# Optimization experiments

Measured on AMD Instinct MI355X. Metric: run time of the kernel, lower is better.

Reference implementation:

```python
import jax, jax.numpy as jnp
import numpy as np
from jax import lax

DIM = 768
SLICES = 12
HEADS = 16
P = 8                      # window_size
CS = DIM // SLICES         # channels per group = 64
HD = DIM // HEADS          # head_dim = 48
BLK = HD // SLICES         # mask block = 4


def group_norm(x, w, b, groups, eps=1e-5):
    # torch GroupNorm: normalize over (C//groups, H, W) per group, biased var
    B, C, H, W = x.shape
    xg = x.reshape(B, groups, (C // groups) * H * W)
    mu = xg.mean(axis=2, keepdims=True)
    var = xg.var(axis=2, keepdims=True)
    xn = ((xg - mu) * lax.rsqrt(var + eps)).reshape(B, C, H, W)
    return xn * w[None, :, None, None] + b[None, :, None, None]


def gconv1x1(x, w, b, groups):
    # grouped 1x1 conv == block-diagonal matmul over channel groups
    B, C, H, W = x.shape
    Co = w.shape[0]
    xg = x.reshape(B, groups, C // groups, H * W)
    wg = w.reshape(groups, Co // groups, C // groups)
    out = jnp.einsum('goi,bgin->bgon', wg, xg).reshape(B, Co, H, W)
    return out + b[None, :, None, None]


def dwconv3(x, w, b):
    # depthwise 3x3, padding 1 (SAME)
    out = lax.conv_general_dilated(x, w, (1, 1), 'SAME',
                                   feature_group_count=x.shape[1],
                                   dimension_numbers=('NCHW', 'OIHW', 'NCHW'))
    return out + b[None, :, None, None]


def gelu(x):
    return jax.nn.gelu(x, approximate=False)  # torch nn.GELU default = exact erf


def tca_forward(y, norm1_w, norm1_b, cpe_w, cpe_b, cpe_nw, cpe_nb,
                qw, qb, kw, kb, vw, vb, pw, pb,
                norm2_w, norm2_b, f1w, f1b, f2w, f2b):
    B, C, H, W = y.shape
    w1, w2 = H // P, W // P
    # window partition: b c (w1 p1) (w2 p2) -> (b w1 w2) c p1 p2
    yw = y.reshape(B, C, w1, P, w2, P).transpose(0, 2, 4, 1, 3, 5).reshape(B * w1 * w2, C, P, P)
    yn = group_norm(yw, norm1_w, norm1_b, SLICES)
    # ConvPosEnc: x + gelu(groupnorm(dwconv(x)))
    feat = group_norm(dwconv3(yn, cpe_w, cpe_b), cpe_nw, cpe_nb, SLICES)
    yn = yn + gelu(feat)
    q = gconv1x1(yn, qw, qb, SLICES)
    k = gconv1x1(yn, kw, kb, SLICES)
    v = gconv1x1(yn, vw, vb, SLICES)
    Bp = yn.shape[0]
    N = P * P
    # torch view(B,N,C//h,h): channel c = d*HEADS + head  ->  (Bp, HD, HEADS, N)
    def split(t):
        return t.reshape(Bp, HD, HEADS, N).transpose(0, 2, 1, 3)  # (Bp, h, hd, N)
    qh, kh, vh = split(q), split(k), split(v)
    scale = HD ** -0.5
    attn = jnp.einsum('bhdn,bhen->bhde', qh * scale, kh)  # channel-attention: (hd x hd)
    idx = jnp.arange(HD)
    mask = (idx[None, :] // BLK) > (idx[:, None] // BLK)  # block-causal over channel slices
    attn = jnp.where(mask[None, None], -jnp.inf, attn)
    attn = jax.nn.softmax(attn, axis=-1)
    out = jnp.einsum('bhde,bhen->bhdn', attn, vh)
    out = out.transpose(0, 2, 1, 3).reshape(Bp, C, P, P)  # back to c = d*HEADS + head
    out = gconv1x1(out, pw, pb, SLICES)
    # window reverse
    out = out.reshape(B, w1, w2, C, P, P).transpose(0, 3, 1, 4, 2, 5).reshape(B, C, H, W)
    tgt = y + out
    t2 = group_norm(tgt, norm2_w, norm2_b, SLICES)
    t2 = gconv1x1(gelu(gconv1x1(t2, f1w, f1b, SLICES)), f2w, f2b, SLICES)
    return tgt + t2


def setup_inputs():
    key = jax.random.key(0)
    ks = jax.random.split(key, 9)
    B, H, W = 2, 256, 256
    f32 = jnp.float32
    d = {}
    d['y'] = jax.random.normal(ks[0], (B, DIM, H, W), f32)
    d['norm1_w'] = jnp.ones((DIM,), f32); d['norm1_b'] = jnp.zeros((DIM,), f32)
    d['cpe_w'] = jax.random.normal(ks[1], (DIM, 1, 3, 3), f32) * 0.1
    d['cpe_b'] = jnp.zeros((DIM,), f32)
    d['cpe_nw'] = jnp.ones((DIM,), f32); d['cpe_nb'] = jnp.zeros((DIM,), f32)
    d['qw'] = jax.random.normal(ks[2], (DIM, CS), f32) * 0.05; d['qb'] = jnp.zeros((DIM,), f32)
    d['kw'] = jax.random.normal(ks[3], (DIM, CS), f32) * 0.05; d['kb'] = jnp.zeros((DIM,), f32)
    d['vw'] = jax.random.normal(ks[4], (DIM, CS), f32) * 0.05; d['vb'] = jnp.zeros((DIM,), f32)
    d['pw'] = jax.random.normal(ks[5], (DIM, CS), f32) * 0.05; d['pb'] = jnp.zeros((DIM,), f32)
    d['norm2_w'] = jnp.ones((DIM,), f32); d['norm2_b'] = jnp.zeros((DIM,), f32)
    d['f1w'] = jax.random.normal(ks[6], (DIM, CS), f32) * 0.05; d['f1b'] = jnp.zeros((DIM,), f32)
    d['f2w'] = jax.random.normal(ks[7], (DIM, CS), f32) * 0.05; d['f2b'] = jnp.zeros((DIM,), f32)
    return d


def reference(y, norm1_w, norm1_b, cpe_w, cpe_b, cpe_nw, cpe_nb,
              qw, qb, kw, kb, vw, vb, pw, pb,
              norm2_w, norm2_b, f1w, f1b, f2w, f2b):
    return tca_forward(y, norm1_w, norm1_b, cpe_w, cpe_b, cpe_nw, cpe_nb,
                       qw, qb, kw, kb, vw, vb, pw, pb,
                       norm2_w, norm2_b, f1w, f1b, f2w, f2b)
```

## Files before the change

kernel.cpp:

```cpp
#include <hip/hip_runtime.h>
#include <hip/hip_bf16.h>

#define IMG 256
#define NPOS 65536

typedef __attribute__((ext_vector_type(8))) short short8;
typedef __attribute__((ext_vector_type(4))) float f32x4;

__device__ __forceinline__ float gelu_exact(float x){
  return 0.5f * x * (1.0f + erff(x * 0.7071067811865475f));
}

__device__ __forceinline__ short f2b(float x){
  __hip_bfloat16 hh = __float2bfloat16(x);
  short s;
  __builtin_memcpy(&s, &hh, sizeof(s));
  return s;
}

__device__ __forceinline__ float b2f(short s){
  unsigned int u = ((unsigned int)(unsigned short)s) << 16;
  float f;
  __builtin_memcpy(&f, &u, sizeof(f));
  return f;
}

template<int NWAVES>
__device__ __forceinline__ void block_reduce2(float& s, float& s2, float* red){
  __syncthreads();
  #pragma unroll
  for (int off=32; off>0; off>>=1){ s += __shfl_down(s, off); s2 += __shfl_down(s2, off); }
  int lane = threadIdx.x & 63, w = threadIdx.x >> 6;
  if (lane==0){ red[w*2]=s; red[w*2+1]=s2; }
  __syncthreads();
  if (threadIdx.x==0){
    float a=0.f, bb=0.f;
    #pragma unroll
    for (int i=0;i<NWAVES;i++){ a+=red[i*2]; bb+=red[i*2+1]; }
    red[2*NWAVES]=a; red[2*NWAVES+1]=bb;
  }
  __syncthreads();
  s=red[2*NWAVES]; s2=red[2*NWAVES+1];
}

__global__ __launch_bounds__(1024) void w_cvt(
    const float* __restrict__ w0, const float* __restrict__ w1,
    const float* __restrict__ w2, const float* __restrict__ w3,
    const float* __restrict__ w4, const float* __restrict__ w5,
    short* __restrict__ outw)
{
  const int mi = blockIdx.y;
  const float* src = mi==0?w0: mi==1?w1: mi==2?w2: mi==3?w3: mi==4?w4: w5;
  const int i = blockIdx.x*1024 + threadIdx.x;
  outw[(size_t)mi*49152 + i] = f2b(src[i]);
}

__global__ __launch_bounds__(1024) void k_abcp(
    const float* __restrict__ y,
    const float* __restrict__ n1w, const float* __restrict__ n1b,
    const float* __restrict__ cw,  const float* __restrict__ cb,
    const float* __restrict__ cnw, const float* __restrict__ cnb,
    const short* __restrict__ qwB, const float* __restrict__ qb,
    const short* __restrict__ kwB, const float* __restrict__ kb,
    const short* __restrict__ vwB, const float* __restrict__ vb,
    const short* __restrict__ pwB, const float* __restrict__ pb,
    short* __restrict__ qG, short* __restrict__ kG, short* __restrict__ vG,
    float* __restrict__ out, float* __restrict__ part, int win0)
{
  extern __shared__ short SM[];
  char* SMb = (char*)SM;

  const int t = threadIdx.x;
  const int bid = blockIdx.x;
  const int nwq = gridDim.x >> 3;
  const int wl  = (bid & 7) * nwq + (bid >> 3);
  const int win = win0 + wl;
  const int b = win>>10, W1=(win>>5)&31, W2=win&31;
  const size_t ybase = (size_t)b*768*(size_t)NPOS + (size_t)(W1*8)*IMG + (W2*8);

  const int h = t>>6, ln = t&63;
  const int l15 = ln&15, c4 = ln>>4, kb8 = c4*8, rbase = c4*4;

  if (h < 12){
    const int g = h;
    const int p1 = ln>>3, p2 = ln&7;
    const bool up = p1>0, dn = p1<7, lt = p2>0, rt = p2<7;
    const float* yg = y + ybase + (size_t)(g*64)*NPOS + (size_t)p1*IMG + p2;
    const int swzofs = (ln&7)<<4;
    char* slotbase = SMb + ln*1536;

    float s=0.f, s2=0.f;
    #pragma unroll
    for (int c0=0;c0<64;c0+=8){
      short8 pk;
      #pragma unroll
      for (int j=0;j<8;++j){
        float v = yg[(size_t)(c0+j)*NPOS];
        s += v; s2 += v*v;
        pk[j] = f2b(v);
      }
      *(short8*)(slotbase + ((g*128 + c0*2) ^ swzofs)) = pk;
    }
    #pragma unroll
    for (int off=32; off>0; off>>=1){ s += __shfl_xor(s, off); s2 += __shfl_xor(s2, off); }
    const float mean = s * (1.f/4096.f);
    const float rstd = rsqrtf(s2*(1.f/4096.f) - mean*mean + 1e-5f);

    float sc=0.f, sc2=0.f;
    #pragma unroll 1
    for (int c0=0;c0<64;c0+=8){
      short8 y8 = *(const short8*)(slotbase + ((g*128 + c0*2) ^ swzofs));
      #pragma unroll
      for (int j=0;j<8;++j){
        const int cg = g*64 + c0 + j;
        float a = n1w[cg]*rstd;
        float x = fmaf(b2f(y8[j]), a, n1b[cg] - mean*a);
        float nmm = __shfl(x, (ln-9)&63);
        float nm0 = __shfl(x, (ln-8)&63);
        float nmp = __shfl(x, (ln-7)&63);
        float n0m = __shfl(x, (ln-1)&63);
        float n0p = __shfl(x, (ln+1)&63);
        float npm = __shfl(x, (ln+7)&63);
        float np0 = __shfl(x, (ln+8)&63);
        float npp = __shfl(x, (ln+9)&63);
        const float* wp = cw + cg*9;
        float acc = cb[cg];
        acc = fmaf(wp[0], (up&&lt)?nmm:0.f, acc);
        acc = fmaf(wp[1], up?nm0:0.f, acc);
        acc = fmaf(wp[2], (up&&rt)?nmp:0.f, acc);
        acc = fmaf(wp[3], lt?n0m:0.f, acc);
        acc = fmaf(wp[4], x, acc);
        acc = fmaf(wp[5], rt?n0p:0.f, acc);
        acc = fmaf(wp[6], (dn&&lt)?npm:0.f, acc);
        acc = fmaf(wp[7], dn?np0:0.f, acc);
        acc = fmaf(wp[8], (dn&&rt)?npp:0.f, acc);
        sc += acc; sc2 += acc*acc;
      }
    }
    #pragma unroll
    for (int off=32; off>0; off>>=1){ sc += __shfl_xor(sc, off); sc2 += __shfl_xor(sc2, off); }
    const float mean2 = sc * (1.f/4096.f);
    const float rstd2 = rsqrtf(sc2*(1.f/4096.f) - mean2*mean2 + 1e-5f);

    #pragma unroll 1
    for (int c0=0;c0<64;c0+=8){
      short8 y8 = *(const short8*)(slotbase + ((g*128 + c0*2) ^ swzofs));
      short8 o8;
      #pragma unroll
      for (int j=0;j<8;++j){
        const int cg = g*64 + c0 + j;
        float a = n1w[cg]*rstd;
        float x = fmaf(b2f(y8[j]), a, n1b[cg] - mean*a);
        float nmm = __shfl(x, (ln-9)&63);
        float nm0 = __shfl(x, (ln-8)&63);
        float nmp = __shfl(x, (ln-7)&63);
        float n0m = __shfl(x, (ln-1)&63);
        float n0p = __shfl(x, (ln+1)&63);
        float npm = __shfl(x, (ln+7)&63);
        float np0 = __shfl(x, (ln+8)&63);
        float npp = __shfl(x, (ln+9)&63);
        const float* wp = cw + cg*9;
        float acc = cb[cg];
        acc = fmaf(wp[0], (up&&lt)?nmm:0.f, acc);
        acc = fmaf(wp[1], up?nm0:0.f, acc);
        acc = fmaf(wp[2], (up&&rt)?nmp:0.f, acc);
        acc = fmaf(wp[3], lt?n0m:0.f, acc);
        acc = fmaf(wp[4], x, acc);
        acc = fmaf(wp[5], rt?n0p:0.f, acc);
        acc = fmaf(wp[6], (dn&&lt)?npm:0.f, acc);
        acc = fmaf(wp[7], dn?np0:0.f, acc);
        acc = fmaf(wp[8], (dn&&rt)?npp:0.f, acc);
        float f = (acc - mean2)*rstd2*cnw[cg] + cnb[cg];
        o8[j] = f2b(x + gelu_exact(f));
      }
      *(short8*)(slotbase + ((g*128 + c0*2) ^ swzofs)) = o8;
    }
  }
  __syncthreads();

  for (int u = h; u < 36; u += 16){
    const int mat = (u<12)?0:((u<24)?1:2);
    const int g = u - mat*12;
    const short* WB = mat==0?qwB:(mat==1?kwB:vwB);
    const float* Bb = mat==0?qb:(mat==1?kb:vb);
    short* dst = mat==0?qG:(mat==1?kG:vG);
    short8 afr[4][2];
    float bias[4][4];
    #pragma unroll
    for (int mt2=0;mt2<4;++mt2){
      #pragma unroll
      for (int ks=0;ks<2;++ks)
        afr[mt2][ks] = *(const short8*)&WB[(size_t)(g*64+mt2*16+l15)*64 + ks*32 + kb8];
      #pragma unroll
      for (int r=0;r<4;++r)
        bias[mt2][r] = Bb[g*64 + mt2*16 + rbase + r];
    }
    #pragma unroll
    for (int nt=0;nt<4;++nt){
      const int pos = nt*16 + l15;
      short8 b0 = *(const short8*)(SMb + pos*1536 + ((g*128 +      kb8*2) ^ ((pos&7)<<4)));
      short8 b1 = *(const short8*)(SMb + pos*1536 + ((g*128 + 64 + kb8*2) ^ ((pos&7)<<4)));
      #pragma unroll
      for (int mt2=0;mt2<4;++mt2){
        f32x4 acc = {0.f,0.f,0.f,0.f};
        acc = __builtin_amdgcn_mfma_f32_16x16x32_bf16(afr[mt2][0], b0, acc, 0,0,0);
        acc = __builtin_amdgcn_mfma_f32_16x16x32_bf16(afr[mt2][1], b1, acc, 0,0,0);
        #pragma unroll
        for (int r=0;r<4;++r){
          const int hh = rbase + r;
          float val = acc[r] + bias[mt2][r];
          size_t addr = ((size_t)(wl*16 + hh)*48 + 4*g + mt2)*64 + pos;
          dst[addr] = f2b(mat==0 ? val * 0.14433756729740643f : val);
        }
      }
    }
  }

  __threadfence_block();
  __syncthreads();

  const size_t hbase = (size_t)(wl*16+h)*48;
  short* R = SM + h*4096;

  short8 kf[3][2], qf[3][2];
  #pragma unroll
  for (int tt=0;tt<3;++tt)
    #pragma unroll
    for (int ks=0;ks<2;++ks){
      kf[tt][ks] = *(const short8*)&kG[(hbase + 16*tt + l15)*64 + ks*32 + kb8];
      qf[tt][ks] = *(const short8*)&qG[(hbase + 16*tt + l15)*64 + ks*32 + kb8];
    }
  f32x4 Su[6];
  const int DTa[6] = {0,1,1,2,2,2};
  const int ETa[6] = {0,0,1,0,1,2};
  #pragma unroll
  for (int u=0;u<6;++u){
    f32x4 acc = {0.f,0.f,0.f,0.f};
    acc = __builtin_amdgcn_mfma_f32_16x16x32_bf16(kf[ETa[u]][0], qf[DTa[u]][0], acc, 0,0,0);
    acc = __builtin_amdgcn_mfma_f32_16x16x32_bf16(kf[ETa[u]][1], qf[DTa[u]][1], acc, 0,0,0);
    Su[u] = acc;
  }

  float inv3[3];
  #pragma unroll
  for (int dt=0;dt<3;++dt){
    const int ub = (dt==0)?0:((dt==1)?1:3);
    float m = -1e30f;
    #pragma unroll
    for (int et=0; et<=dt; ++et)
      #pragma unroll
      for (int r=0;r<4;++r){
        bool valid = (et<dt) || ((rbase + r) <= (l15|3));
        if (valid) m = fmaxf(m, Su[ub+et][r]);
      }
    m = fmaxf(m, __shfl_xor(m,16));
    m = fmaxf(m, __shfl_xor(m,32));
    float sm = 0.f;
    #pragma unroll
    for (int et=0; et<=dt; ++et)
      #pragma unroll
      for (int r=0;r<4;++r){
        bool valid = (et<dt) || ((rbase + r) <= (l15|3));
        float p = valid ? expf(Su[ub+et][r] - m) : 0.f;
        Su[ub+et][r] = p; sm += p;
      }
    sm += __shfl_xor(sm,16);
    sm += __shfl_xor(sm,32);
    inv3[dt] = 1.f/sm;
  }

  short8 z8 = {0,0,0,0,0,0,0,0};
  #pragma unroll
  for (int nblk=0;nblk<8;++nblk){
    short8 v8 = z8;
    if (ln < 48) v8 = *(const short8*)&vG[(hbase + ln)*64 + nblk*8];
    #pragma unroll
    for (int j=0;j<8;++j){
      int n = nblk*8 + j;
      R[n*64 + (((ln>>3) ^ (n&7))<<3) + (ln&7)] = v8[j];
    }
  }
  short8 bv[4][2];
  #pragma unroll
  for (int nt=0;nt<4;++nt){
    const int n = 16*nt + l15;
    bv[nt][0] = *(const short8*)&R[n*64 + ((c4 ^ (n&7))<<3)];
    bv[nt][1] = *(const short8*)&R[n*64 + (((4+c4) ^ (n&7))<<3)];
  }

  #pragma unroll
  for (int i_=0;i_<6;++i_) *(short8*)&R[i_*512 + ln*8] = z8;
  #pragma unroll
  for (int dt=0;dt<3;++dt){
    const int ub = (dt==0)?0:((dt==1)?1:3);
    const int d = 16*dt + l15;
    #pragma unroll
    for (int et=0; et<=dt; ++et)
      #pragma unroll
      for (int r=0;r<4;++r){
        int e = 16*et + rbase + r;
        R[d*64 + (((e>>3) ^ (d&7))<<3) + (e&7)] = f2b(Su[ub+et][r]*inv3[dt]);
      }
  }
  short8 aP[4];
  const int PDT[4] = {0,1,2,2}, PKS[4] = {0,0,0,1};
  #pragma unroll
  for (int i_=0;i_<4;++i_){
    int d = 16*PDT[i_] + l15;
    int ch = PKS[i_]*4 + c4;
    aP[i_] = *(const short8*)&R[d*64 + ((ch ^ (d&7))<<3)];
  }

  __syncthreads();

  #pragma unroll
  for (int nt=0;nt<4;++nt){
    const int n = 16*nt + l15;
    f32x4 O0 = {0.f,0.f,0.f,0.f};
    f32x4 O1 = {0.f,0.f,0.f,0.f};
    f32x4 O2 = {0.f,0.f,0.f,0.f};
    O0 = __builtin_amdgcn_mfma_f32_16x16x32_bf16(aP[0], bv[nt][0], O0, 0,0,0);
    O1 = __builtin_amdgcn_mfma_f32_16x16x32_bf16(aP[1], bv[nt][0], O1, 0,0,0);
    O2 = __builtin_amdgcn_mfma_f32_16x16x32_bf16(aP[2], bv[nt][0], O2, 0,0,0);
    O2 = __builtin_amdgcn_mfma_f32_16x16x32_bf16(aP[3], bv[nt][1], O2, 0,0,0);
    #pragma unroll
    for (int r=0;r<4;++r){
      const int swz = (((2*r + (h>>3)) ^ (n&7))<<3) + (h&7);
      SM[(c4     )*4096 + n*64 + swz] = f2b(O0[r]);
      SM[(4 + c4 )*4096 + n*64 + swz] = f2b(O1[r]);
      SM[(8 + c4 )*4096 + n*64 + swz] = f2b(O2[r]);
    }
  }

  __syncthreads();

  #pragma unroll 1
  for (int j=0;j<3;++j){
    const int u = h*3 + j;
    const int g = u>>2, mt = u&3;
    short8 aw[2];
    float bi[4];
    #pragma unroll
    for (int ks=0;ks<2;++ks)
      aw[ks] = *(const short8*)&pwB[(size_t)(g*64 + mt*16 + l15)*64 + ks*32 + kb8];
    #pragma unroll
    for (int r=0;r<4;++r) bi[r] = pb[g*64 + mt*16 + rbase + r];

    f32x4 acc[4] = {};
    #pragma unroll
    for (int nt=0;nt<4;++nt){
      const int n = 16*nt + l15;
      short8 b0 = *(const short8*)&SM[g*4096 + n*64 + ((c4 ^ (n&7))<<3)];
      short8 b1 = *(const short8*)&SM[g*4096 + n*64 + (((4+c4) ^ (n&7))<<3)];
      acc[nt] = __builtin_amdgcn_mfma_f32_16x16x32_bf16(aw[0], b0, acc[nt], 0,0,0);
      acc[nt] = __builtin_amdgcn_mfma_f32_16x16x32_bf16(aw[1], b1, acc[nt], 0,0,0);
    }
    float s=0.f, s2=0.f;
    #pragma unroll
    for (int nt=0;nt<4;++nt){
      const int n = 16*nt + l15;
      const size_t rowoff = ybase + (size_t)(n>>3)*IMG + (n&7);
      #pragma unroll
      for (int r=0;r<4;++r){
        int m = mt*16 + rbase + r;
        size_t ad = rowoff + (size_t)(g*64+m)*NPOS;
        float o = y[ad] + bi[r] + acc[nt][r];
        out[ad] = o;
        s += o; s2 += o*o;
      }
    }
    #pragma unroll
    for (int off=32; off>0; off>>=1){ s += __shfl_xor(s, off); s2 += __shfl_xor(s2, off); }
    if (ln==0){
      size_t idx = ((size_t)(b*12+g)*1024 + (win&1023))*4 + mt;
      part[idx*2+0]=s; part[idx*2+1]=s2;
    }
  }
}

__global__ __launch_bounds__(256) void k3_stats(
    const float* __restrict__ part, float* __restrict__ stats)
{
  const int bg = blockIdx.x;
  const int t = threadIdx.x;
  float s=0.f, s2=0.f;
  #pragma unroll
  for (int j=0;j<16;++j){
    size_t idx = (size_t)bg*4096 + t*16 + j;
    s  += part[idx*2+0];
    s2 += part[idx*2+1];
  }
  __shared__ float red[10];
  block_reduce2<4>(s,s2,red);
  if (t==0){
    const float Ninv = 1.f/(64.f*65536.f);
    float mean = s*Ninv;
    float var  = s2*Ninv - mean*mean;
    stats[bg*2+0] = mean;
    stats[bg*2+1] = rsqrtf(var + 1e-5f);
  }
}

__global__ __launch_bounds__(256) void k_d(
    const float* __restrict__ n2w, const float* __restrict__ n2b,
    const short* __restrict__ f1wB, const float* __restrict__ f1b,
    const short* __restrict__ f2wB, const float* __restrict__ f2bi,
    const float* __restrict__ stats, float* __restrict__ io)
{
  __shared__ short Xb[4096];
  __shared__ short Hb[4096];
  const int t = threadIdx.x;
  const int pt = blockIdx.x, g = blockIdx.y, b = blockIdx.z;
  const int bg = b*12 + g;
  const float mean = stats[bg*2+0], rstd = stats[bg*2+1];
  const size_t base = ((size_t)(b*768 + g*64))*NPOS + (size_t)pt*64;

  const int wv = t>>6, ln = t&63;
  const int l15 = ln&15, kb8 = (ln>>4)*8, rbase = (ln>>4)*4, c4 = ln>>4;
  const int n = wv*16 + l15;

  float res[16];
  #pragma unroll
  for (int mt=0;mt<4;++mt)
    #pragma unroll
    for (int r=0;r<4;++r)
      res[mt*4+r] = io[base + (size_t)(mt*16 + rbase + r)*NPOS + n];

  {
    const int pp = t>>3, posq = t&7;
    const int ch0 = pp*2;
    const float* p0 = io + base + (size_t)ch0*NPOS + posq*8;
    float4 x00 = *(const float4*)p0;
    float4 x01 = *(const float4*)(p0+4);
    const float* p1 = p0 + NPOS;
    float4 x10 = *(const float4*)p1;
    float4 x11 = *(const float4*)(p1+4);
    float A0 = rstd*n2w[g*64+ch0],   C0 = n2b[g*64+ch0]   - mean*A0;
    float A1 = rstd*n2w[g*64+ch0+1], C1 = n2b[g*64+ch0+1] - mean*A1;
    float va[8] = {x00.x,x00.y,x00.z,x00.w,x01.x,x01.y,x01.z,x01.w};
    float vb[8] = {x10.x,x10.y,x10.z,x10.w,x11.x,x11.y,x11.z,x11.w};
    #pragma unroll
    for (int j=0;j<8;++j){
      int pos = posq*8 + j;
      unsigned int u0 = (unsigned short)f2b(va[j]*A0 + C0);
      unsigned int u1 = (unsigned short)f2b(vb[j]*A1 + C1);
      *(unsigned int*)&Xb[pos*64 + (((ch0>>3) ^ (pos&7))<<3) + (ch0&7)] = u0 | (u1<<16);
    }
  }
  __syncthreads();

  short8 af[4][2];
  #pragma unroll
  for (int mt=0;mt<4;++mt)
    #pragma unroll
    for (int ks=0;ks<2;++ks)
      af[mt][ks] = *(const short8*)&f1wB[(size_t)(g*64 + mt*16 + l15)*64 + ks*32 + kb8];
  f32x4 h[4] = {};
  #pragma unroll
  for (int ks=0;ks<2;++ks){
    short8 bfr = *(const short8*)&Xb[n*64 + (((ks*4 + c4) ^ (n&7))<<3)];
    #pragma unroll
    for (int mt=0;mt<4;++mt)
      h[mt] = __builtin_amdgcn_mfma_f32_16x16x32_bf16(af[mt][ks], bfr, h[mt], 0,0,0);
  }
  #pragma unroll
  for (int mt=0;mt<4;++mt){
    #pragma unroll
    for (int rp=0;rp<4;rp+=2){
      int m = mt*16 + rbase + rp;
      float h0 = gelu_exact(h[mt][rp]   + f1b[g*64+m]);
      float h1 = gelu_exact(h[mt][rp+1] + f1b[g*64+m+1]);
      unsigned int u0 = (unsigned short)f2b(h0);
      unsigned int u1 = (unsigned short)f2b(h1);
      *(unsigned int*)&Hb[n*64 + (((m>>3) ^ (n&7))<<3) + (m&7)] = u0 | (u1<<16);
    }
  }
  __syncthreads();

  #pragma unroll
  for (int mt=0;mt<4;++mt)
    #pragma unroll
    for (int ks=0;ks<2;++ks)
      af[mt][ks] = *(const short8*)&f2wB[(size_t)(g*64 + mt*16 + l15)*64 + ks*32 + kb8];
  f32x4 o[4] = {};
  #pragma unroll
  for (int ks=0;ks<2;++ks){
    short8 bfr = *(const short8*)&Hb[n*64 + (((ks*4 + c4) ^ (n&7))<<3)];
    #pragma unroll
    for (int mt=0;mt<4;++mt)
      o[mt] = __builtin_amdgcn_mfma_f32_16x16x32_bf16(af[mt][ks], bfr, o[mt], 0,0,0);
  }
  #pragma unroll
  for (int mt=0;mt<4;++mt)
    #pragma unroll
    for (int r=0;r<4;++r){
      int m = mt*16 + rbase + r;
      io[base + (size_t)m*NPOS + n] = res[mt*4+r] + o[mt][r] + f2bi[g*64+m];
    }
}

extern "C" void kernel_launch(void* const* d_in, const int* in_sizes, int n_in,
                              void* d_out, int out_size, void* d_ws, size_t ws_size,
                              hipStream_t stream){
  const float* y    = (const float*)d_in[0];
  const float* n1w  = (const float*)d_in[1];
  const float* n1b  = (const float*)d_in[2];
  const float* cw   = (const float*)d_in[3];
  const float* cb   = (const float*)d_in[4];
  const float* cnw  = (const float*)d_in[5];
  const float* cnb  = (const float*)d_in[6];
  const float* qw   = (const float*)d_in[7];
  const float* qb   = (const float*)d_in[8];
  const float* kw   = (const float*)d_in[9];
  const float* kb   = (const float*)d_in[10];
  const float* vw   = (const float*)d_in[11];
  const float* vb   = (const float*)d_in[12];
  const float* pw   = (const float*)d_in[13];
  const float* pb   = (const float*)d_in[14];
  const float* n2w  = (const float*)d_in[15];
  const float* n2b  = (const float*)d_in[16];
  const float* f1w  = (const float*)d_in[17];
  const float* f1b  = (const float*)d_in[18];
  const float* f2w  = (const float*)d_in[19];
  const float* f2b_ = (const float*)d_in[20];
  float* out   = (float*)d_out;

  unsigned char* wsb = (unsigned char*)d_ws;
  float* part  = (float*)wsb;
  float* stats = part + 24*1024*4*2;
  short* wbf   = (short*)(wsb + 786624);
  short* qwB  = wbf;
  short* kwB  = wbf + 49152;
  short* vwB  = wbf + 2*49152;
  short* pwB  = wbf + 3*49152;
  short* f1wB = wbf + 4*49152;
  short* f2wB = wbf + 5*49152;

  int C = 32;
  {
    const int cand[6] = {1,2,4,8,16,32};
    for (int i=0;i<6;++i){
      int nw = 2048 / cand[i];
      size_t Y = (size_t)nw * 16 * 48 * 64 * 2;
      if ((size_t)(1<<21) + 3*Y <= ws_size){ C = cand[i]; break; }
    }
  }
  const int nw = 2048 / C;
  const size_t Y = (size_t)nw * 16 * 48 * 64 * 2;
  short* qG  = (short*)(wsb + (1<<21));
  short* kG  = (short*)(wsb + (1<<21) + Y);
  short* vG  = (short*)(wsb + (1<<21) + 2*Y);

  hipLaunchKernelGGL(w_cvt, dim3(48, 6), dim3(1024), 0, stream,
                     qw, kw, vw, pw, f1w, f2w, wbf);

  for (int c=0; c<C; ++c){
    int win0 = c * nw;
    hipLaunchKernelGGL(k_abcp, dim3(nw), dim3(1024), 131072, stream,
                       y, n1w,n1b, cw,cb, cnw,cnb,
                       qwB,qb, kwB,kb, vwB,vb, pwB,pb,
                       qG, kG, vG, out, part, win0);
  }
  hipLaunchKernelGGL(k3_stats, dim3(24), dim3(256), 0, stream, part, stats);
  hipLaunchKernelGGL(k_d, dim3(1024, 12, 2), dim3(256), 0, stream,
                     n2w,n2b, f1wB,f1b, f2wB,f2b_, stats, out);
}
```

Before: 1.402 ms.

## Split fused window kernel into per-group QKV kernel and attention kernel

New measurement: 1.315 ms. 6.3% less time.

```diff
diff --git a/kernel.cpp b/kernel.cpp
--- a/kernel.cpp
+++ b/kernel.cpp
@@ -55,7 +55,7 @@
   outw[(size_t)mi*49152 + i] = f2b(src[i]);
 }
 
-__global__ __launch_bounds__(1024) void k_abcp(
+__global__ __launch_bounds__(256) void k_ab(
     const float* __restrict__ y,
     const float* __restrict__ n1w, const float* __restrict__ n1b,
     const float* __restrict__ cw,  const float* __restrict__ cb,
@@ -63,31 +63,27 @@
     const short* __restrict__ qwB, const float* __restrict__ qb,
     const short* __restrict__ kwB, const float* __restrict__ kb,
     const short* __restrict__ vwB, const float* __restrict__ vb,
-    const short* __restrict__ pwB, const float* __restrict__ pb,
     short* __restrict__ qG, short* __restrict__ kG, short* __restrict__ vG,
-    float* __restrict__ out, float* __restrict__ part, int win0)
+    int win0)
 {
-  extern __shared__ short SM[];
-  char* SMb = (char*)SM;
-
+  __shared__ char SMB[32768];
   const int t = threadIdx.x;
+  const int w = t>>6, ln = t&63;
   const int bid = blockIdx.x;
   const int nwq = gridDim.x >> 3;
   const int wl  = (bid & 7) * nwq + (bid >> 3);
   const int win = win0 + wl;
   const int b = win>>10, W1=(win>>5)&31, W2=win&31;
   const size_t ybase = (size_t)b*768*(size_t)NPOS + (size_t)(W1*8)*IMG + (W2*8);
-
-  const int h = t>>6, ln = t&63;
-  const int l15 = ln&15, c4 = ln>>4, kb8 = c4*8, rbase = c4*4;
-
-  if (h < 12){
-    const int g = h;
+  const int g = blockIdx.y*4 + w;
+  char* region = SMB + w*8192;
+
+  {
     const int p1 = ln>>3, p2 = ln&7;
     const bool up = p1>0, dn = p1<7, lt = p2>0, rt = p2<7;
     const float* yg = y + ybase + (size_t)(g*64)*NPOS + (size_t)p1*IMG + p2;
     const int swzofs = (ln&7)<<4;
-    char* slotbase = SMb + ln*1536;
+    char* slotbase = region + ln*128;
 
     float s=0.f, s2=0.f;
     #pragma unroll
@@ -99,7 +95,7 @@
         s += v; s2 += v*v;
         pk[j] = f2b(v);
       }
-      *(short8*)(slotbase + ((g*128 + c0*2) ^ swzofs)) = pk;
+      *(short8*)(slotbase + ((c0*2) ^ swzofs)) = pk;
     }
     #pragma unroll
     for (int off=32; off>0; off>>=1){ s += __shfl_xor(s, off); s2 += __shfl_xor(s2, off); }
@@ -109,7 +105,7 @@
     float sc=0.f, sc2=0.f;
     #pragma unroll 1
     for (int c0=0;c0<64;c0+=8){
-      short8 y8 = *(const short8*)(slotbase + ((g*128 + c0*2) ^ swzofs));
+      short8 y8 = *(const short8*)(slotbase + ((c0*2) ^ swzofs));
       #pragma unroll
       for (int j=0;j<8;++j){
         const int cg = g*64 + c0 + j;
@@ -144,7 +140,7 @@
 
     #pragma unroll 1
     for (int c0=0;c0<64;c0+=8){
-      short8 y8 = *(const short8*)(slotbase + ((g*128 + c0*2) ^ swzofs));
+      short8 y8 = *(const short8*)(slotbase + ((c0*2) ^ swzofs));
       short8 o8;
       #pragma unroll
       for (int j=0;j<8;++j){
@@ -173,14 +169,13 @@
         float f = (acc - mean2)*rstd2*cnw[cg] + cnb[cg];
         o8[j] = f2b(x + gelu_exact(f));
       }
-      *(short8*)(slotbase + ((g*128 + c0*2) ^ swzofs)) = o8;
-    }
-  }
-  __syncthreads();
-
-  for (int u = h; u < 36; u += 16){
-    const int mat = (u<12)?0:((u<24)?1:2);
-    const int g = u - mat*12;
+      *(short8*)(slotbase + ((c0*2) ^ swzofs)) = o8;
+    }
+  }
+
+  const int l15 = ln&15, c4 = ln>>4, kb8 = c4*8, rbase = c4*4;
+  #pragma unroll 1
+  for (int mat=0; mat<3; ++mat){
     const short* WB = mat==0?qwB:(mat==1?kwB:vwB);
     const float* Bb = mat==0?qb:(mat==1?kb:vb);
     short* dst = mat==0?qG:(mat==1?kG:vG);
@@ -198,8 +193,8 @@
     #pragma unroll
     for (int nt=0;nt<4;++nt){
       const int pos = nt*16 + l15;
-      short8 b0 = *(const short8*)(SMb + pos*1536 + ((g*128 +      kb8*2) ^ ((pos&7)<<4)));
-      short8 b1 = *(const short8*)(SMb + pos*1536 + ((g*128 + 64 + kb8*2) ^ ((pos&7)<<4)));
+      short8 b0 = *(const short8*)(region + pos*128 + ((      kb8*2) ^ ((pos&7)<<4)));
+      short8 b1 = *(const short8*)(region + pos*128 + ((64 + kb8*2) ^ ((pos&7)<<4)));
       #pragma unroll
       for (int mt2=0;mt2<4;++mt2){
         f32x4 acc = {0.f,0.f,0.f,0.f};
@@ -215,10 +210,25 @@
       }
     }
   }
-
-  __threadfence_block();
-  __syncthreads();
-
+}
+
+__global__ __launch_bounds__(1024) void k_cp(
+    const short* __restrict__ qG, const short* __restrict__ kG,
+    const short* __restrict__ vG,
+    const float* __restrict__ y,
+    const short* __restrict__ pwB, const float* __restrict__ pb,
+    float* __restrict__ out, float* __restrict__ part, int win0)
+{
+  extern __shared__ short SM[];
+  const int t = threadIdx.x;
+  const int h = t>>6, ln = t&63;
+  const int bid = blockIdx.x;
+  const int nwq = gridDim.x >> 3;
+  const int wl  = (bid & 7) * nwq + (bid >> 3);
+  const int win = win0 + wl;
+  const int b = win>>10, W1=(win>>5)&31, W2=win&31;
+  const size_t ybase = (size_t)b*768*(size_t)NPOS + (size_t)(W1*8)*IMG + (W2*8);
+  const int l15 = ln&15, c4 = ln>>4, kb8 = c4*8, rbase = c4*4;
   const size_t hbase = (size_t)(wl*16+h)*48;
   short* R = SM + h*4096;
 
@@ -538,8 +548,8 @@
 
   int C = 32;
   {
-    const int cand[6] = {1,2,4,8,16,32};
-    for (int i=0;i<6;++i){
+    const int cand[4] = {4,8,16,32};
+    for (int i=0;i<4;++i){
       int nw = 2048 / cand[i];
       size_t Y = (size_t)nw * 16 * 48 * 64 * 2;
       if ((size_t)(1<<21) + 3*Y <= ws_size){ C = cand[i]; break; }
@@ -556,10 +566,12 @@
 
   for (int c=0; c<C; ++c){
     int win0 = c * nw;
-    hipLaunchKernelGGL(k_abcp, dim3(nw), dim3(1024), 131072, stream,
+    hipLaunchKernelGGL(k_ab, dim3(nw, 3), dim3(256), 0, stream,
                        y, n1w,n1b, cw,cb, cnw,cnb,
-                       qwB,qb, kwB,kb, vwB,vb, pwB,pb,
-                       qG, kG, vG, out, part, win0);
+                       qwB,qb, kwB,kb, vwB,vb,
+                       qG, kG, vG, win0);
+    hipLaunchKernelGGL(k_cp, dim3(nw), dim3(1024), 131072, stream,
+                       qG, kG, vG, y, pwB, pb, out, part, win0);
   }
   hipLaunchKernelGGL(k3_stats, dim3(24), dim3(256), 0, stream, part, stats);
   hipLaunchKernelGGL(k_d, dim3(1024, 12, 2), dim3(256), 0, stream,
```
